# Optimization experiments

Measured on AMD Instinct MI355X. Metric: run time of the kernel, lower is better.

Reference implementation:

```python
import jax, jax.numpy as jnp
import numpy as np

N = 50000      # nodes
E = 600000     # edges (avg degree 12)
D = 128        # input_dim == hidden_dim (required: same Linear reused across pool layers)
OUT = 64       # output_dim
NUM_POOL = 2   # num_pool_layers


def setup_inputs() -> dict:
    key = jax.random.key(0)
    ks = jax.random.split(key, 8)
    s = 1.0 / np.sqrt(D)  # fan-in style scaling keeps repeated scatter-adds stable
    x = jax.random.normal(ks[0], (N, D), dtype=jnp.float32)
    edge_index = jax.random.randint(ks[1], (2, E), 0, N, dtype=jnp.int64)
    W1 = jax.random.normal(ks[2], (D, D), dtype=jnp.float32) * s
    b1 = jnp.zeros((D,), dtype=jnp.float32)
    W2 = jax.random.normal(ks[3], (D, D), dtype=jnp.float32) * s
    b2 = jnp.zeros((D,), dtype=jnp.float32)
    Wout = jax.random.normal(ks[4], (D, OUT), dtype=jnp.float32) * s
    bout = jnp.zeros((OUT,), dtype=jnp.float32)
    return {"x": x, "edge_index": edge_index, "W1": W1, "b1": b1,
            "W2": W2, "b2": b2, "Wout": Wout, "bout": bout}


def _gauss_seidel_pool(x, W, b, src, dst, num_layers):
    # PyG MessagePassing(aggr='add'): out[i] = sum_{edges (j->i)} lin(x[j]).
    # Nodes with no incoming edges become zero (propagate replaces x entirely).
    for _ in range(num_layers):
        m = x @ W + b                      # [N, out] linear once per node (== lin(x_j) per edge)
        x = jax.ops.segment_sum(m[src], dst, num_segments=N)  # gather + scatter-add
    return x


def reference(x, edge_index, W1, b1, W2, b2, Wout, bout):
    src = edge_index[0]  # x_j source
    dst = edge_index[1]  # aggregation target i
    h = _gauss_seidel_pool(x, W1, b1, src, dst, NUM_POOL)
    h = jax.nn.relu(h)                     # dropout = identity (eval mode)
    h = _gauss_seidel_pool(h, W2, b2, src, dst, NUM_POOL)
    h = jax.nn.relu(h)
    return h @ Wout + bout                 # [N, OUT]
```

## Files before the change

kernel.cpp:

```cpp
#include <hip/hip_runtime.h>


static inline int ceil_div(int a, int b) { return (a + b - 1) / b; }

typedef __attribute__((ext_vector_type(8))) short bf16x8;
typedef __attribute__((ext_vector_type(4))) float f32x4;

__device__ inline unsigned short f2bf(float f) {
    unsigned u = __float_as_uint(f);
    return (unsigned short)((u + 0x7fffu + ((u >> 16) & 1u)) >> 16);
}


__device__ void wprep_dev(const float* __restrict__ W, unsigned short* __restrict__ hi,
                          int total, int C, int g0, int G) {
    for (int t = g0; t < total; t += G) {
        int j = t & 7;
        int lane = (t >> 3) & 63;
        int f = t >> 9;
        int c = f & 3, ct = f >> 2;
        int k = c * 32 + (lane >> 4) * 8 + j;
        int col = ct * 16 + (lane & 15);
        hi[t] = f2bf(W[(size_t)k * C + col]);
    }
}

__global__ __launch_bounds__(256) void prep_kernel(const float* __restrict__ x,
                                                   const float* __restrict__ W1,
                                                   const float* __restrict__ W2,
                                                   const float* __restrict__ Wout,
                                                   unsigned short* __restrict__ xb,
                                                   unsigned short* __restrict__ W1hi,
                                                   unsigned short* __restrict__ W2hi,
                                                   unsigned short* __restrict__ Wohi,
                                                   int* __restrict__ cursor,
                                                   unsigned* __restrict__ stat,
                                                   int N, int nChunks) {
    int g0 = blockIdx.x * 256 + threadIdx.x;
    int G = gridDim.x * 256;
    for (int i = g0; i < N; i += G) cursor[i] = 0;
    for (int i = g0; i < nChunks; i += G) stat[i] = 0;

    int nq = N * 32;
    for (int i = g0; i < nq; i += G) {
        float4 v = ((const float4*)x)[i];
        ushort4 o;
        o.x = f2bf(v.x); o.y = f2bf(v.y); o.z = f2bf(v.z); o.w = f2bf(v.w);
        ((ushort4*)xb)[i] = o;
    }

    wprep_dev(W1, W1hi, 128 * 128, 128, g0, G);
    wprep_dev(W2, W2hi, 128 * 128, 128, g0, G);
    wprep_dev(Wout, Wohi, 128 * 64, 64, g0, G);
}


__global__ __launch_bounds__(256) void hist_kernel(const int* __restrict__ dst,
                                                   int* __restrict__ deg, int E) {
    int e = blockIdx.x * 256 + threadIdx.x;
    if (e < E) atomicAdd(&deg[dst[e]], 1);
}

__global__ __launch_bounds__(256) void scan_fuse_kernel(const int* __restrict__ deg,
                                                        int* __restrict__ rp,
                                                        int* __restrict__ cursor,
                                                        unsigned* __restrict__ stat,
                                                        int N) {
    __shared__ int s[256];
    int c = blockIdx.x, tid = threadIdx.x;
    int i = c * 256 + tid;
    int v = (i < N) ? deg[i] : 0;
    s[tid] = v;
    __syncthreads();
    for (int off = 1; off < 256; off <<= 1) {
        int t = (tid >= off) ? s[tid - off] : 0;
        __syncthreads();
        s[tid] += t;
        __syncthreads();
    }
    int loc = s[tid] - v;
    int tot = s[255];
    __syncthreads();
    if (tid == 0) atomicExch(&stat[c], (unsigned)tot | 0x80000000u);

    unsigned mine = 0;
    if (tid < c) {
        unsigned u;
        do { u = atomicAdd(&stat[tid], 0u); } while (!(u & 0x80000000u));
        mine = u & 0x7fffffffu;
    }
    s[tid] = (int)mine;
    __syncthreads();
    for (int off = 128; off >= 1; off >>= 1) {
        if (tid < off) s[tid] += s[tid + off];
        __syncthreads();
    }
    int prefix = s[0];
    if (i <= N) {
        int val = loc + prefix;
        rp[i] = val;
        if (i < N) cursor[i] = val;
    }
}

__global__ __launch_bounds__(256) void fill_kernel(const int* __restrict__ src,
                                                   const int* __restrict__ dst,
                                                   int* __restrict__ cursor,
                                                   unsigned short* __restrict__ es, int E) {
    int e = blockIdx.x * 256 + threadIdx.x;
    if (e < E) {
        int p = atomicAdd(&cursor[dst[e]], 1);
        es[p] = (unsigned short)src[e];
    }
}


__device__ inline void acc_row4(float* a, uint2 v) {
    a[0] += __uint_as_float(v.x << 16);
    a[1] += __uint_as_float(v.x & 0xffff0000u);
    a[2] += __uint_as_float(v.y << 16);
    a[3] += __uint_as_float(v.y & 0xffff0000u);
}

template <bool RELU, bool OUTCHAIN>
__global__ __launch_bounds__(256) void fused_kernel(const unsigned short* __restrict__ M,
                                                    const int* __restrict__ rp,
                                                    const unsigned short* __restrict__ es,
                                                    const uint4* __restrict__ Whi,
                                                    const float* __restrict__ bvec,
                                                    const uint4* __restrict__ Wof,
                                                    const float* __restrict__ bout,
                                                    void* __restrict__ Yv, int n) {
    constexpr int SR = 136;
    constexpr int ECAP = 1280;
    __shared__ unsigned short Hl[64 * SR];
    __shared__ unsigned short esl[ECAP];
    __shared__ int rpl[65];
    __shared__ unsigned char perm[64];

    int tid = threadIdx.x;
    int r0 = blockIdx.x * 64;

    if (tid < 65) {
        int gi = r0 + tid;
        if (gi > n) gi = n;
        rpl[tid] = rp[gi];
    }
    __syncthreads();

    int ebase = rpl[0];
    int ecnt = rpl[64] - ebase;
    if (ecnt > ECAP) ecnt = ECAP;

    if (tid < 64) {
        int di = rpl[tid + 1] - rpl[tid];
        int rank = 0;
        for (int j = 0; j < 64; ++j) {
            int dj = rpl[j + 1] - rpl[j];
            rank += (dj > di) || (dj == di && j < tid);
        }
        perm[rank] = (unsigned char)tid;
    }
    for (int i = tid; i < ecnt; i += 256) esl[i] = es[ebase + i];
    __syncthreads();

    {
        int g = tid >> 4, ln = tid & 15;
#pragma unroll 1
        for (int half = 0; half < 2; ++half) {
            const unsigned short* Mh = M + half * 64 + ln * 4;
#pragma unroll 1
            for (int q = 0; q < 4; ++q) {
                int nl = perm[q * 16 + g];
                int pbeg = rpl[nl] - ebase, pend = rpl[nl + 1] - ebase;
                int pm = pend < ecnt ? pend : ecnt;
                float acc[4] = {};
                int p = pbeg;
                for (; p + 8 <= pm; p += 8) {
                    int s0 = esl[p],     s1 = esl[p + 1], s2 = esl[p + 2], s3 = esl[p + 3];
                    int s4 = esl[p + 4], s5 = esl[p + 5], s6 = esl[p + 6], s7 = esl[p + 7];
                    uint2 v0 = *(const uint2*)(Mh + (size_t)s0 * 128);
                    uint2 v1 = *(const uint2*)(Mh + (size_t)s1 * 128);
                    uint2 v2 = *(const uint2*)(Mh + (size_t)s2 * 128);
                    uint2 v3 = *(const uint2*)(Mh + (size_t)s3 * 128);
                    uint2 v4 = *(const uint2*)(Mh + (size_t)s4 * 128);
                    uint2 v5 = *(const uint2*)(Mh + (size_t)s5 * 128);
                    uint2 v6 = *(const uint2*)(Mh + (size_t)s6 * 128);
                    uint2 v7 = *(const uint2*)(Mh + (size_t)s7 * 128);
                    acc_row4(acc, v0); acc_row4(acc, v1);
                    acc_row4(acc, v2); acc_row4(acc, v3);
                    acc_row4(acc, v4); acc_row4(acc, v5);
                    acc_row4(acc, v6); acc_row4(acc, v7);
                }
                for (; p + 4 <= pm; p += 4) {
                    int s0 = esl[p], s1 = esl[p + 1], s2 = esl[p + 2], s3 = esl[p + 3];
                    uint2 v0 = *(const uint2*)(Mh + (size_t)s0 * 128);
                    uint2 v1 = *(const uint2*)(Mh + (size_t)s1 * 128);
                    uint2 v2 = *(const uint2*)(Mh + (size_t)s2 * 128);
                    uint2 v3 = *(const uint2*)(Mh + (size_t)s3 * 128);
                    acc_row4(acc, v0); acc_row4(acc, v1);
                    acc_row4(acc, v2); acc_row4(acc, v3);
                }
                for (; p < pm; ++p) {
                    uint2 v = *(const uint2*)(Mh + (size_t)esl[p] * 128);
                    acc_row4(acc, v);
                }
                for (; p < pend; ++p) {
                    uint2 v = *(const uint2*)(Mh + (size_t)es[ebase + p] * 128);
                    acc_row4(acc, v);
                }
                uint2 o;
                o.x = (unsigned)f2bf(acc[0]) | ((unsigned)f2bf(acc[1]) << 16);
                o.y = (unsigned)f2bf(acc[2]) | ((unsigned)f2bf(acc[3]) << 16);
                *(uint2*)(&Hl[nl * SR + half * 64 + ln * 4]) = o;
            }
        }
    }
    __syncthreads();

    int wave = tid >> 6, lane = tid & 63;
    int lm = lane & 15, lq = lane >> 4;

    f32x4 acc[4][2];
#pragma unroll
    for (int rt = 0; rt < 4; ++rt)
#pragma unroll
        for (int t = 0; t < 2; ++t)
            acc[rt][t] = (f32x4){0.f, 0.f, 0.f, 0.f};

#pragma unroll
    for (int c = 0; c < 4; ++c) {
        bf16x8 afr[4];
#pragma unroll
        for (int rt = 0; rt < 4; ++rt)
            afr[rt] = *(const bf16x8*)(&Hl[(rt * 16 + lm) * SR + c * 32 + lq * 8]);
#pragma unroll
        for (int t = 0; t < 2; ++t) {
            int ct = wave * 2 + t;
            uint4 uh = Whi[(ct * 4 + c) * 64 + lane];
            bf16x8 wh = *(const bf16x8*)&uh;
#pragma unroll
            for (int rt = 0; rt < 4; ++rt)
                acc[rt][t] = __builtin_amdgcn_mfma_f32_16x16x32_bf16(afr[rt], wh, acc[rt][t], 0, 0, 0);
        }
    }

    if (!OUTCHAIN) {
#pragma unroll
        for (int t = 0; t < 2; ++t) {
            int col = (wave * 2 + t) * 16 + lm;
            float bv = bvec[col];
#pragma unroll
            for (int rt = 0; rt < 4; ++rt) {
#pragma unroll
                for (int r = 0; r < 4; ++r) {
                    int rowl = rt * 16 + lq * 4 + r;
                    int row = r0 + rowl;
                    if (row < n) {
                        float deg = (float)(rpl[rowl + 1] - rpl[rowl]);
                        float v = acc[rt][t][r] + deg * bv;
                        if (RELU) v = fmaxf(v, 0.f);
                        ((unsigned short*)Yv)[(size_t)row * 128 + col] = f2bf(v);
                    }
                }
            }
        }
    } else {
        __syncthreads();
#pragma unroll
        for (int t = 0; t < 2; ++t) {
            int col = (wave * 2 + t) * 16 + lm;
            float bv = bvec[col];
#pragma unroll
            for (int rt = 0; rt < 4; ++rt) {
#pragma unroll
                for (int r = 0; r < 4; ++r) {
                    int rowl = rt * 16 + lq * 4 + r;
                    float deg = (float)(rpl[rowl + 1] - rpl[rowl]);
                    float v = acc[rt][t][r] + deg * bv;
                    v = fmaxf(v, 0.f);
                    Hl[rowl * SR + col] = f2bf(v);
                }
            }
        }
        __syncthreads();

        f32x4 acc2[4];
#pragma unroll
        for (int rt = 0; rt < 4; ++rt) acc2[rt] = (f32x4){0.f, 0.f, 0.f, 0.f};

#pragma unroll
        for (int c = 0; c < 4; ++c) {
            bf16x8 afr[4];
#pragma unroll
            for (int rt = 0; rt < 4; ++rt)
                afr[rt] = *(const bf16x8*)(&Hl[(rt * 16 + lm) * SR + c * 32 + lq * 8]);
            uint4 uw = Wof[(wave * 4 + c) * 64 + lane];
            bf16x8 wf = *(const bf16x8*)&uw;
#pragma unroll
            for (int rt = 0; rt < 4; ++rt)
                acc2[rt] = __builtin_amdgcn_mfma_f32_16x16x32_bf16(afr[rt], wf, acc2[rt], 0, 0, 0);
        }

        int col = wave * 16 + lm;
        float bo = bout[col];
#pragma unroll
        for (int rt = 0; rt < 4; ++rt) {
#pragma unroll
            for (int r = 0; r < 4; ++r) {
                int row = r0 + rt * 16 + lq * 4 + r;
                if (row < n)
                    ((float*)Yv)[(size_t)row * 64 + col] = acc2[rt][r] + bo;
            }
        }
    }
}


extern "C" void kernel_launch(void* const* d_in, const int* in_sizes, int n_in,
                              void* d_out, int out_size, void* d_ws, size_t ws_size,
                              hipStream_t stream) {
    const float* x    = (const float*)d_in[0];
    const int*   ei   = (const int*)d_in[1];
    const float* W1   = (const float*)d_in[2];
    const float* b1   = (const float*)d_in[3];
    const float* W2   = (const float*)d_in[4];
    const float* b2   = (const float*)d_in[5];
    const float* Wout = (const float*)d_in[6];
    const float* bout = (const float*)d_in[7];
    float*       out  = (float*)d_out;

    const int N = in_sizes[0] / 128;
    const int E = in_sizes[1] / 2;
    const int* src = ei;
    const int* dst = ei + E;

    char* ws = (char*)d_ws;
    auto take = [&](size_t bytes) {
        char* p = ws;
        ws += (bytes + 255) & ~(size_t)255;
        return p;
    };
    unsigned short* xb = (unsigned short*)take((size_t)N * 128 * 2);
    unsigned short* mA = (unsigned short*)take((size_t)N * 128 * 2);
    unsigned short* mB = (unsigned short*)take((size_t)N * 128 * 2);
    unsigned short* W1hi = (unsigned short*)take(128 * 128 * 2);
    unsigned short* W2hi = (unsigned short*)take(128 * 128 * 2);
    unsigned short* Wohi = (unsigned short*)take(128 * 64 * 2);
    int* rp      = (int*)take((size_t)(N + 1) * sizeof(int));
    int* cursor  = (int*)take((size_t)N * sizeof(int));
    unsigned short* es = (unsigned short*)take((size_t)E * sizeof(unsigned short));
    unsigned* stat = (unsigned*)take(4096);

    const int nChunks = ceil_div(N + 1, 256);
    const int tiles64 = ceil_div(N, 64);

    prep_kernel<<<256, 256, 0, stream>>>(x, W1, W2, Wout, xb, W1hi, W2hi, Wohi,
                                         cursor, stat, N, nChunks);
    hist_kernel<<<ceil_div(E, 256), 256, 0, stream>>>(dst, cursor, E);
    scan_fuse_kernel<<<nChunks, 256, 0, stream>>>(cursor, rp, cursor, stat, N);
    fill_kernel<<<ceil_div(E, 256), 256, 0, stream>>>(src, dst, cursor, es, E);

    fused_kernel<false, false><<<tiles64, 256, 0, stream>>>(
        xb, rp, es, (const uint4*)W1hi, b1, nullptr, nullptr, mA, N);
    fused_kernel<true, false><<<tiles64, 256, 0, stream>>>(
        mA, rp, es, (const uint4*)W1hi, b1, nullptr, nullptr, mB, N);
    fused_kernel<false, false><<<tiles64, 256, 0, stream>>>(
        mB, rp, es, (const uint4*)W2hi, b2, nullptr, nullptr, mA, N);
    fused_kernel<true, true><<<tiles64, 256, 0, stream>>>(
        mA, rp, es, (const uint4*)W2hi, b2, (const uint4*)Wohi, bout, out, N);
}
```

Before: 279.4 us.

## Split fused aggregate-GEMM into GEMM-first then column-slab gather passes

Reorders each layer so the linear transform runs first and writes its output in 8 column slabs of 16 features. A separate gather pass then handles one slab per block, so each slab (about 1.6 MB) fits in cache while random neighbor rows are gathered. The gather kernel prefetches its slab with a dummy load and writes results with nontemporal stores. The cost is more kernel launches (9 instead of 4) and a full round trip of the intermediate through global memory; the gather work per block is also re-split across 64 nodes times 4 lanes.

```diff
diff --git a/kernel.cpp b/kernel.cpp
--- a/kernel.cpp
+++ b/kernel.cpp
@@ -115,6 +115,54 @@
 }
 
 
+__global__ __launch_bounds__(256) void gemm_pass(const unsigned short* __restrict__ A,
+                                                 const uint4* __restrict__ Whi,
+                                                 unsigned short* __restrict__ Ys,
+                                                 int n, int N) {
+    int tid = threadIdx.x;
+    int r0 = blockIdx.x * 64;
+    int wave = tid >> 6, lane = tid & 63;
+    int lm = lane & 15, lq = lane >> 4;
+
+    f32x4 acc[4][2];
+#pragma unroll
+    for (int rt = 0; rt < 4; ++rt)
+#pragma unroll
+        for (int t = 0; t < 2; ++t)
+            acc[rt][t] = (f32x4){0.f, 0.f, 0.f, 0.f};
+
+#pragma unroll
+    for (int c = 0; c < 4; ++c) {
+        bf16x8 afr[4];
+#pragma unroll
+        for (int rt = 0; rt < 4; ++rt)
+            afr[rt] = *(const bf16x8*)(A + (size_t)(r0 + rt * 16 + lm) * 128 + c * 32 + lq * 8);
+#pragma unroll
+        for (int t = 0; t < 2; ++t) {
+            uint4 uh = Whi[((wave * 2 + t) * 4 + c) * 64 + lane];
+            bf16x8 wh = *(const bf16x8*)&uh;
+#pragma unroll
+            for (int rt = 0; rt < 4; ++rt)
+                acc[rt][t] = __builtin_amdgcn_mfma_f32_16x16x32_bf16(afr[rt], wh, acc[rt][t], 0, 0, 0);
+        }
+    }
+
+#pragma unroll
+    for (int t = 0; t < 2; ++t) {
+        int s = wave * 2 + t;
+#pragma unroll
+        for (int rt = 0; rt < 4; ++rt) {
+#pragma unroll
+            for (int r = 0; r < 4; ++r) {
+                int row = r0 + rt * 16 + lq * 4 + r;
+                if (row < n)
+                    Ys[(size_t)s * N * 16 + (size_t)row * 16 + lm] = f2bf(acc[rt][t][r]);
+            }
+        }
+    }
+}
+
+
 __device__ inline void acc_row4(float* a, uint2 v) {
     a[0] += __uint_as_float(v.x << 16);
     a[1] += __uint_as_float(v.x & 0xffff0000u);
@@ -122,24 +170,32 @@
     a[3] += __uint_as_float(v.y & 0xffff0000u);
 }
 
-template <bool RELU, bool OUTCHAIN>
-__global__ __launch_bounds__(256) void fused_kernel(const unsigned short* __restrict__ M,
-                                                    const int* __restrict__ rp,
-                                                    const unsigned short* __restrict__ es,
-                                                    const uint4* __restrict__ Whi,
-                                                    const float* __restrict__ bvec,
-                                                    const uint4* __restrict__ Wof,
-                                                    const float* __restrict__ bout,
-                                                    void* __restrict__ Yv, int n) {
-    constexpr int SR = 136;
+template <bool RELU>
+__global__ __launch_bounds__(256) void gather_pass(const unsigned short* __restrict__ Ys,
+                                                   const int* __restrict__ rp,
+                                                   const unsigned short* __restrict__ es,
+                                                   const float* __restrict__ bvec,
+                                                   unsigned short* __restrict__ Mout,
+                                                   int n, int N) {
     constexpr int ECAP = 1280;
-    __shared__ unsigned short Hl[64 * SR];
     __shared__ unsigned short esl[ECAP];
     __shared__ int rpl[65];
     __shared__ unsigned char perm[64];
 
     int tid = threadIdx.x;
-    int r0 = blockIdx.x * 64;
+    int s = blockIdx.x & 7;
+    int t = blockIdx.x >> 3;
+    int r0 = t * 64;
+
+    const unsigned short* slab = Ys + (size_t)s * N * 16;
+
+    {
+        int widx = t * 256 + tid;
+        if (widx * 8 < N * 16) {
+            uint4 w = ((const uint4*)slab)[widx];
+            asm volatile("" :: "v"(w.x), "v"(w.y), "v"(w.z), "v"(w.w));
+        }
+    }
 
     if (tid < 65) {
         int gi = r0 + tid;
@@ -164,154 +220,102 @@
     for (int i = tid; i < ecnt; i += 256) esl[i] = es[ebase + i];
     __syncthreads();
 
-    {
-        int g = tid >> 4, ln = tid & 15;
-#pragma unroll 1
-        for (int half = 0; half < 2; ++half) {
-            const unsigned short* Mh = M + half * 64 + ln * 4;
-#pragma unroll 1
-            for (int q = 0; q < 4; ++q) {
-                int nl = perm[q * 16 + g];
-                int pbeg = rpl[nl] - ebase, pend = rpl[nl + 1] - ebase;
-                int pm = pend < ecnt ? pend : ecnt;
-                float acc[4] = {};
-                int p = pbeg;
-                for (; p + 8 <= pm; p += 8) {
-                    int s0 = esl[p],     s1 = esl[p + 1], s2 = esl[p + 2], s3 = esl[p + 3];
-                    int s4 = esl[p + 4], s5 = esl[p + 5], s6 = esl[p + 6], s7 = esl[p + 7];
-                    uint2 v0 = *(const uint2*)(Mh + (size_t)s0 * 128);
-                    uint2 v1 = *(const uint2*)(Mh + (size_t)s1 * 128);
-                    uint2 v2 = *(const uint2*)(Mh + (size_t)s2 * 128);
-                    uint2 v3 = *(const uint2*)(Mh + (size_t)s3 * 128);
-                    uint2 v4 = *(const uint2*)(Mh + (size_t)s4 * 128);
-                    uint2 v5 = *(const uint2*)(Mh + (size_t)s5 * 128);
-                    uint2 v6 = *(const uint2*)(Mh + (size_t)s6 * 128);
-                    uint2 v7 = *(const uint2*)(Mh + (size_t)s7 * 128);
-                    acc_row4(acc, v0); acc_row4(acc, v1);
-                    acc_row4(acc, v2); acc_row4(acc, v3);
-                    acc_row4(acc, v4); acc_row4(acc, v5);
-                    acc_row4(acc, v6); acc_row4(acc, v7);
-                }
-                for (; p + 4 <= pm; p += 4) {
-                    int s0 = esl[p], s1 = esl[p + 1], s2 = esl[p + 2], s3 = esl[p + 3];
-                    uint2 v0 = *(const uint2*)(Mh + (size_t)s0 * 128);
-                    uint2 v1 = *(const uint2*)(Mh + (size_t)s1 * 128);
-                    uint2 v2 = *(const uint2*)(Mh + (size_t)s2 * 128);
-                    uint2 v3 = *(const uint2*)(Mh + (size_t)s3 * 128);
-                    acc_row4(acc, v0); acc_row4(acc, v1);
-                    acc_row4(acc, v2); acc_row4(acc, v3);
-                }
-                for (; p < pm; ++p) {
-                    uint2 v = *(const uint2*)(Mh + (size_t)esl[p] * 128);
-                    acc_row4(acc, v);
-                }
-                for (; p < pend; ++p) {
-                    uint2 v = *(const uint2*)(Mh + (size_t)es[ebase + p] * 128);
-                    acc_row4(acc, v);
-                }
-                uint2 o;
-                o.x = (unsigned)f2bf(acc[0]) | ((unsigned)f2bf(acc[1]) << 16);
-                o.y = (unsigned)f2bf(acc[2]) | ((unsigned)f2bf(acc[3]) << 16);
-                *(uint2*)(&Hl[nl * SR + half * 64 + ln * 4]) = o;
-            }
-        }
-    }
-    __syncthreads();
-
+    int gid = tid >> 2, ln = tid & 3;
+    int nl = perm[gid];
+    int beg = rpl[nl], end = rpl[nl + 1];
+    int pbeg = beg - ebase, pend = end - ebase;
+    int pm = pend < ecnt ? pend : ecnt;
+    const unsigned short* base = slab + ln * 4;
+
+    float a[4] = {};
+    int p = pbeg;
+    for (; p + 8 <= pm; p += 8) {
+        int s0 = esl[p],     s1 = esl[p + 1], s2 = esl[p + 2], s3 = esl[p + 3];
+        int s4 = esl[p + 4], s5 = esl[p + 5], s6 = esl[p + 6], s7 = esl[p + 7];
+        uint2 v0 = *(const uint2*)(base + (size_t)s0 * 16);
+        uint2 v1 = *(const uint2*)(base + (size_t)s1 * 16);
+        uint2 v2 = *(const uint2*)(base + (size_t)s2 * 16);
+        uint2 v3 = *(const uint2*)(base + (size_t)s3 * 16);
+        uint2 v4 = *(const uint2*)(base + (size_t)s4 * 16);
+        uint2 v5 = *(const uint2*)(base + (size_t)s5 * 16);
+        uint2 v6 = *(const uint2*)(base + (size_t)s6 * 16);
+        uint2 v7 = *(const uint2*)(base + (size_t)s7 * 16);
+        acc_row4(a, v0); acc_row4(a, v1); acc_row4(a, v2); acc_row4(a, v3);
+        acc_row4(a, v4); acc_row4(a, v5); acc_row4(a, v6); acc_row4(a, v7);
+    }
+    for (; p + 4 <= pm; p += 4) {
+        int s0 = esl[p], s1 = esl[p + 1], s2 = esl[p + 2], s3 = esl[p + 3];
+        uint2 v0 = *(const uint2*)(base + (size_t)s0 * 16);
+        uint2 v1 = *(const uint2*)(base + (size_t)s1 * 16);
+        uint2 v2 = *(const uint2*)(base + (size_t)s2 * 16);
+        uint2 v3 = *(const uint2*)(base + (size_t)s3 * 16);
+        acc_row4(a, v0); acc_row4(a, v1); acc_row4(a, v2); acc_row4(a, v3);
+    }
+    for (; p < pm; ++p) {
+        uint2 v = *(const uint2*)(base + (size_t)esl[p] * 16);
+        acc_row4(a, v);
+    }
+    for (; p < pend; ++p) {
+        uint2 v = *(const uint2*)(base + (size_t)es[ebase + p] * 16);
+        acc_row4(a, v);
+    }
+
+    int node = r0 + nl;
+    if (node < n) {
+        float deg = (float)(end - beg);
+        float4 bv = *(const float4*)(bvec + s * 16 + ln * 4);
+        float v0 = a[0] + deg * bv.x;
+        float v1 = a[1] + deg * bv.y;
+        float v2 = a[2] + deg * bv.z;
+        float v3 = a[3] + deg * bv.w;
+        if (RELU) {
+            v0 = fmaxf(v0, 0.f); v1 = fmaxf(v1, 0.f);
+            v2 = fmaxf(v2, 0.f); v3 = fmaxf(v3, 0.f);
+        }
+        unsigned lo = (unsigned)f2bf(v0) | ((unsigned)f2bf(v1) << 16);
+        unsigned hi = (unsigned)f2bf(v2) | ((unsigned)f2bf(v3) << 16);
+        unsigned long long o = (unsigned long long)lo | ((unsigned long long)hi << 32);
+        __builtin_nontemporal_store(
+            o, (unsigned long long*)(Mout + (size_t)node * 128 + s * 16 + ln * 4));
+    }
+}
+
+
+__global__ __launch_bounds__(256) void gemm_out(const unsigned short* __restrict__ A,
+                                                const uint4* __restrict__ Wof,
+                                                const float* __restrict__ bout,
+                                                float* __restrict__ out, int n) {
+    int tid = threadIdx.x;
+    int r0 = blockIdx.x * 64;
     int wave = tid >> 6, lane = tid & 63;
     int lm = lane & 15, lq = lane >> 4;
 
-    f32x4 acc[4][2];
-#pragma unroll
-    for (int rt = 0; rt < 4; ++rt)
-#pragma unroll
-        for (int t = 0; t < 2; ++t)
-            acc[rt][t] = (f32x4){0.f, 0.f, 0.f, 0.f};
+    f32x4 acc[4];
+#pragma unroll
+    for (int rt = 0; rt < 4; ++rt) acc[rt] = (f32x4){0.f, 0.f, 0.f, 0.f};
 
 #pragma unroll
     for (int c = 0; c < 4; ++c) {
         bf16x8 afr[4];
 #pragma unroll
         for (int rt = 0; rt < 4; ++rt)
-            afr[rt] = *(const bf16x8*)(&Hl[(rt * 16 + lm) * SR + c * 32 + lq * 8]);
-#pragma unroll
-        for (int t = 0; t < 2; ++t) {
-            int ct = wave * 2 + t;
-            uint4 uh = Whi[(ct * 4 + c) * 64 + lane];
-            bf16x8 wh = *(const bf16x8*)&uh;
-#pragma unroll
-            for (int rt = 0; rt < 4; ++rt)
-                acc[rt][t] = __builtin_amdgcn_mfma_f32_16x16x32_bf16(afr[rt], wh, acc[rt][t], 0, 0, 0);
-        }
-    }
-
-    if (!OUTCHAIN) {
-#pragma unroll
-        for (int t = 0; t < 2; ++t) {
-            int col = (wave * 2 + t) * 16 + lm;
-            float bv = bvec[col];
-#pragma unroll
-            for (int rt = 0; rt < 4; ++rt) {
-#pragma unroll
-                for (int r = 0; r < 4; ++r) {
-                    int rowl = rt * 16 + lq * 4 + r;
-                    int row = r0 + rowl;
-                    if (row < n) {
-                        float deg = (float)(rpl[rowl + 1] - rpl[rowl]);
-                        float v = acc[rt][t][r] + deg * bv;
-                        if (RELU) v = fmaxf(v, 0.f);
-                        ((unsigned short*)Yv)[(size_t)row * 128 + col] = f2bf(v);
-                    }
-                }
-            }
-        }
-    } else {
-        __syncthreads();
-#pragma unroll
-        for (int t = 0; t < 2; ++t) {
-            int col = (wave * 2 + t) * 16 + lm;
-            float bv = bvec[col];
-#pragma unroll
-            for (int rt = 0; rt < 4; ++rt) {
-#pragma unroll
-                for (int r = 0; r < 4; ++r) {
-                    int rowl = rt * 16 + lq * 4 + r;
-                    float deg = (float)(rpl[rowl + 1] - rpl[rowl]);
-                    float v = acc[rt][t][r] + deg * bv;
-                    v = fmaxf(v, 0.f);
-                    Hl[rowl * SR + col] = f2bf(v);
-                }
-            }
-        }
-        __syncthreads();
-
-        f32x4 acc2[4];
-#pragma unroll
-        for (int rt = 0; rt < 4; ++rt) acc2[rt] = (f32x4){0.f, 0.f, 0.f, 0.f};
-
-#pragma unroll
-        for (int c = 0; c < 4; ++c) {
-            bf16x8 afr[4];
-#pragma unroll
-            for (int rt = 0; rt < 4; ++rt)
-                afr[rt] = *(const bf16x8*)(&Hl[(rt * 16 + lm) * SR + c * 32 + lq * 8]);
-            uint4 uw = Wof[(wave * 4 + c) * 64 + lane];
-            bf16x8 wf = *(const bf16x8*)&uw;
-#pragma unroll
-            for (int rt = 0; rt < 4; ++rt)
-                acc2[rt] = __builtin_amdgcn_mfma_f32_16x16x32_bf16(afr[rt], wf, acc2[rt], 0, 0, 0);
-        }
-
-        int col = wave * 16 + lm;
-        float bo = bout[col];
-#pragma unroll
-        for (int rt = 0; rt < 4; ++rt) {
-#pragma unroll
-            for (int r = 0; r < 4; ++r) {
-                int row = r0 + rt * 16 + lq * 4 + r;
-                if (row < n)
-                    ((float*)Yv)[(size_t)row * 64 + col] = acc2[rt][r] + bo;
-            }
+            afr[rt] = *(const bf16x8*)(A + (size_t)(r0 + rt * 16 + lm) * 128 + c * 32 + lq * 8);
+        uint4 uw = Wof[(wave * 4 + c) * 64 + lane];
+        bf16x8 wf = *(const bf16x8*)&uw;
+#pragma unroll
+        for (int rt = 0; rt < 4; ++rt)
+            acc[rt] = __builtin_amdgcn_mfma_f32_16x16x32_bf16(afr[rt], wf, acc[rt], 0, 0, 0);
+    }
+
+    int col = wave * 16 + lm;
+    float bo = bout[col];
+#pragma unroll
+    for (int rt = 0; rt < 4; ++rt) {
+#pragma unroll
+        for (int r = 0; r < 4; ++r) {
+            int row = r0 + rt * 16 + lq * 4 + r;
+            if (row < n)
+                out[(size_t)row * 64 + col] = acc[rt][r] + bo;
         }
     }
 }
@@ -341,9 +345,9 @@
         ws += (bytes + 255) & ~(size_t)255;
         return p;
     };
-    unsigned short* xb = (unsigned short*)take((size_t)N * 128 * 2);
+    unsigned short* BM = (unsigned short*)take((size_t)N * 128 * 2);
     unsigned short* mA = (unsigned short*)take((size_t)N * 128 * 2);
-    unsigned short* mB = (unsigned short*)take((size_t)N * 128 * 2);
+    unsigned short* Ys = (unsigned short*)take((size_t)N * 128 * 2);
     unsigned short* W1hi = (unsigned short*)take(128 * 128 * 2);
     unsigned short* W2hi = (unsigned short*)take(128 * 128 * 2);
     unsigned short* Wohi = (unsigned short*)take(128 * 64 * 2);
@@ -355,18 +359,19 @@
     const int nChunks = ceil_div(N + 1, 256);
     const int tiles64 = ceil_div(N, 64);
 
-    prep_kernel<<<256, 256, 0, stream>>>(x, W1, W2, Wout, xb, W1hi, W2hi, Wohi,
+    prep_kernel<<<256, 256, 0, stream>>>(x, W1, W2, Wout, BM, W1hi, W2hi, Wohi,
                                          cursor, stat, N, nChunks);
     hist_kernel<<<ceil_div(E, 256), 256, 0, stream>>>(dst, cursor, E);
     scan_fuse_kernel<<<nChunks, 256, 0, stream>>>(cursor, rp, cursor, stat, N);
     fill_kernel<<<ceil_div(E, 256), 256, 0, stream>>>(src, dst, cursor, es, E);
 
-    fused_kernel<false, false><<<tiles64, 256, 0, stream>>>(
-        xb, rp, es, (const uint4*)W1hi, b1, nullptr, nullptr, mA, N);
-    fused_kernel<true, false><<<tiles64, 256, 0, stream>>>(
-        mA, rp, es, (const uint4*)W1hi, b1, nullptr, nullptr, mB, N);
-    fused_kernel<false, false><<<tiles64, 256, 0, stream>>>(
-        mB, rp, es, (const uint4*)W2hi, b2, nullptr, nullptr, mA, N);
-    fused_kernel<true, true><<<tiles64, 256, 0, stream>>>(
-        mA, rp, es, (const uint4*)W2hi, b2, (const uint4*)Wohi, bout, out, N);
-}
+    gemm_pass<<<tiles64, 256, 0, stream>>>(BM, (const uint4*)W1hi, Ys, N, N);
+    gather_pass<false><<<tiles64 * 8, 256, 0, stream>>>(Ys, rp, es, b1, mA, N, N);
+    gemm_pass<<<tiles64, 256, 0, stream>>>(mA, (const uint4*)W1hi, Ys, N, N);
+    gather_pass<true><<<tiles64 * 8, 256, 0, stream>>>(Ys, rp, es, b1, BM, N, N);
+    gemm_pass<<<tiles64, 256, 0, stream>>>(BM, (const uint4*)W2hi, Ys, N, N);
+    gather_pass<false><<<tiles64 * 8, 256, 0, stream>>>(Ys, rp, es, b2, mA, N, N);
+    gemm_pass<<<tiles64, 256, 0, stream>>>(mA, (const uint4*)W2hi, Ys, N, N);
+    gather_pass<true><<<tiles64 * 8, 256, 0, stream>>>(Ys, rp, es, b2, BM, N, N);
+    gemm_out<<<tiles64, 256, 0, stream>>>(BM, (const uint4*)Wohi, bout, out, N);
+}
```

New measurement: 362.2 us. 1.3x slower.
